# Kernel optimization log

Measured on AMD Instinct MI355X. Metric: run time of the kernel, lower is better.

The kernel has to match this reference:

```python
import jax, jax.numpy as jnp
import numpy as np

WS = 17  # window_size


def _conv(x, w, padding, groups=1):
    return jax.lax.conv_general_dilated(
        x, w, window_strides=(1, 1), padding=padding,
        dimension_numbers=("NCHW", "OIHW", "NCHW"),
        feature_group_count=groups)


def setup_inputs() -> dict:
    key = jax.random.key(0)
    ks = jax.random.split(key, 5)
    B, C, H, W = 4, 64, 510, 510
    x = jax.random.normal(ks[0], (B, C, H, W), dtype=jnp.float32)
    # Sobel depthwise kernel, exactly as init_sobel_weights
    sobel = jnp.array([[-1.0, 0.0, 1.0], [-2.0, 0.0, 2.0], [-1.0, 0.0, 1.0]],
                      dtype=jnp.float32)
    sobel_w = jnp.tile(sobel[None, None], (C, 1, 1, 1))  # [C,1,3,3]
    w1 = jax.random.normal(ks[1], (16, C, 3, 3), jnp.float32) * 0.04
    b1 = jax.random.normal(ks[2], (16,), jnp.float32) * 0.01
    w2 = jax.random.normal(ks[3], (1, 16, 1, 1), jnp.float32) * 0.1
    b2 = jax.random.normal(ks[4], (1,), jnp.float32) * 0.01
    return {"x": x, "sobel_w": sobel_w, "w1": w1, "b1": b1, "w2": w2, "b2": b2}


def reference(x, sobel_w, w1, b1, w2, b2):
    B, C, H, W = x.shape
    pad_h = (-H) % WS
    pad_w = (-W) % WS
    x = jnp.pad(x, ((0, 0), (0, 0), (0, pad_h), (0, pad_w)))
    Hp, Wp = H + pad_h, W + pad_w
    nh, nw = Hp // WS, Wp // WS
    # F.unfold with kernel=stride=WS on NCHW == non-overlapping window split.
    # Window order is row-major over (nh, nw), matching unfold's column order.
    xw = (x.reshape(B, C, nh, WS, nw, WS)
           .transpose(0, 2, 4, 1, 3, 5)
           .reshape(B * nh * nw, C, WS, WS))
    # depthwise 3x3 sobel filter, padding=1
    freq = _conv(xw, sobel_w, [(1, 1), (1, 1)], groups=C)
    # mask generator: Conv(C->16,3x3) + ReLU + Conv(16->1,1x1) + Sigmoid
    h = jax.nn.relu(_conv(freq, w1, [(1, 1), (1, 1)]) + b1[None, :, None, None])
    mask = jax.nn.sigmoid(_conv(h, w2, [(0, 0), (0, 0)]) + b2[None, :, None, None])
    mask = jnp.clip(mask, 0.05, 0.95)
    # F.fold with non-overlapping windows; divisor fold(unfold(ones)) == 1,
    # so the divide / nan_to_num are identities.
    attn = (mask.reshape(B, nh, nw, 1, WS, WS)
                .transpose(0, 3, 1, 4, 2, 5)
                .reshape(B, 1, Hp, Wp))
    return attn[:, :, :H, :W]
```

## Files before the change

### kernel.cpp

```cpp
#include <hip/hip_runtime.h>


#define WSZ 17
#define PS  19
#define PSS (PS * PS)
#define NT  512
#define CH  (510 * 510)

typedef __attribute__((ext_vector_type(8))) short bf16x8;
typedef __attribute__((ext_vector_type(4))) float f32x4;
typedef __attribute__((ext_vector_type(2))) float f32x2;

__device__ __forceinline__ int swz(int off) {
    return off ^ (((off >> 7) & 7) << 4);
}

__device__ __forceinline__ unsigned short f2bf(float f) {
    union { float f; unsigned u; } v; v.f = f;
    unsigned u = v.u;
    unsigned r = u + 0x7fffu + ((u >> 16) & 1u);
    return (unsigned short)(r >> 16);
}

__device__ __forceinline__ float dpp_shr1(float v) {
    return __int_as_float(
        __builtin_amdgcn_update_dpp(0, __float_as_int(v), 0x138, 0xf, 0xf, true));
}
__device__ __forceinline__ float dpp_shl1(float v) {
    return __int_as_float(
        __builtin_amdgcn_update_dpp(0, __float_as_int(v), 0x130, 0xf, 0xf, true));
}

__global__ void prep_w1(const float* __restrict__ w1, unsigned short* __restrict__ wt) {
    const int dij = blockIdx.x >> 1;
    const int ks  = blockIdx.x & 1;
    const int l   = threadIdx.x;
    const int m   = l & 15;
    const int kb  = ks * 32 + 8 * (l >> 4);
    bf16x8 v;
#pragma unroll
    for (int jj = 0; jj < 8; ++jj)
        v[jj] = (short)f2bf(w1[m * 576 + (kb + jj) * 9 + dij]);
    ((bf16x8*)wt)[blockIdx.x * 64 + l] = v;
}

__global__ __launch_bounds__(NT, 4)
void fasa_mfma(const float* __restrict__ x,
               const float* __restrict__ sobel_w,
               const unsigned short* __restrict__ wt,
               const float* __restrict__ b1,
               const float* __restrict__ w2,
               const float* __restrict__ b2,
               float* __restrict__ out)
{
    __shared__ __align__(16) char frq[PSS * 128];

    const int t    = threadIdx.x;
    const int lane = t & 63;
    const int wave = __builtin_amdgcn_readfirstlane(t >> 6);

    const int bid = blockIdx.x;
    const int win = (bid & 7) * 450 + (bid >> 3);
    const int b   = win / 900;
    const int rem = win % 900;
    const int h0  = (rem / 30) * WSZ;
    const int w0  = (rem % 30) * WSZ;

    for (int u = t; u < 72 * 8; u += NT) {
        int r = u >> 3, k = u & 7;
        int row;
        if      (r < 19) row = r;
        else if (r < 38) row = 342 + (r - 19);
        else if (r < 55) row = (r - 37) * PS;
        else             row = (r - 54) * PS + 18;
        *(f32x4*)(frq + row * 128 + k * 16) = (f32x4){0.f, 0.f, 0.f, 0.f};
    }

    float sw[9];
#pragma unroll
    for (int k = 0; k < 9; ++k) sw[k] = sobel_w[k];

    const int j   = lane & 31;
    const int grp = lane >> 5;
    const bool jac = (j < 17);

    const float* xbase = x + ((size_t)(b * 64 + 4 * wave)) * CH
                           + (size_t)h0 * 510 + w0;
    const unsigned voffx = (unsigned)((grp * 2 * CH + j) * 4);
    const unsigned voffy = voffx + (unsigned)(CH * 4);

    auto LOADCOL = [&](f32x2* xr, int q) {
        const char* bp = (const char*)(xbase + (size_t)q * 32 * CH);
        xr[0] = (f32x2){0.f, 0.f}; xr[18] = (f32x2){0.f, 0.f};
        if (jac) {
#pragma unroll
            for (int i = 0; i < 17; ++i) {
                xr[i + 1].x = *(const float*)(bp + (voffx + (unsigned)i * 2040u));
                xr[i + 1].y = *(const float*)(bp + (voffy + (unsigned)i * 2040u));
            }
        } else {
#pragma unroll
            for (int i = 0; i < 17; ++i) xr[i + 1] = (f32x2){0.f, 0.f};
        }
    };

    auto DOSOBEL = [&](const f32x2* xr, int q) {
        const int pr = 2 * wave + grp + 16 * q;
        const int pairOff = pr * 4;
#pragma unroll
        for (int i = 0; i < 17; ++i) {
            f32x2 p0 = sw[0] * xr[i] + sw[3] * xr[i + 1] + sw[6] * xr[i + 2];
            f32x2 p1 = sw[1] * xr[i] + sw[4] * xr[i + 1] + sw[7] * xr[i + 2];
            f32x2 p2 = sw[2] * xr[i] + sw[5] * xr[i + 1] + sw[8] * xr[i + 2];
            f32x2 o;
            o.x = p1.x + dpp_shr1(p0.x) + dpp_shl1(p2.x);
            o.y = p1.y + dpp_shr1(p0.y) + dpp_shl1(p2.y);
            unsigned pkv;
            asm("v_cvt_pk_bf16_f32 %0, %1, %2" : "=v"(pkv) : "v"(o.x), "v"(o.y));
            if (jac)
                *(unsigned*)(frq + swz(((i + 1) * PS + (j + 1)) * 128 + pairOff)) = pkv;
        }
    };

    f32x2 A[19], B[19];
    LOADCOL(A, 0);
    LOADCOL(B, 1);
    DOSOBEL(A, 0);
    DOSOBEL(B, 1);

    bf16x8 wf[18];
#pragma unroll
    for (int i = 0; i < 18; ++i)
        wf[i] = ((const bf16x8*)wt)[i * 64 + lane];

    float b1v[4], w2v[4];
#pragma unroll
    for (int r = 0; r < 4; ++r) {
        int m = 4 * (lane >> 4) + r;
        b1v[r] = b1[m];
        w2v[r] = w2[m];
    }
    const float b2v = b2[0];

    __syncthreads();

    const int n   = lane & 15;
    const int g16 = (lane >> 4) * 16;
    const int DOFF[9] = {0, 1, 2, PS, PS + 1, PS + 2, 2 * PS, 2 * PS + 1, 2 * PS + 2};

#pragma unroll 1
    for (int nt = wave; nt < 19; nt += 8) {
        int p  = nt * 16 + n;
        int pv = p > 288 ? 288 : p;
        int pi = pv / 17, pj = pv - pi * 17;
        int base = (pi * PS + pj) * 128 + g16;

        f32x4 acc = {0.f, 0.f, 0.f, 0.f};
#pragma unroll
        for (int d = 0; d < 9; ++d) {
            int off = base + DOFF[d] * 128;
            bf16x8 bfA = *(const bf16x8*)(frq + swz(off));
            bf16x8 bfB = *(const bf16x8*)(frq + swz(off + 64));
            acc = __builtin_amdgcn_mfma_f32_16x16x32_bf16(wf[2 * d],     bfA, acc, 0, 0, 0);
            acc = __builtin_amdgcn_mfma_f32_16x16x32_bf16(wf[2 * d + 1], bfB, acc, 0, 0, 0);
        }

        float part = 0.f;
#pragma unroll
        for (int r = 0; r < 4; ++r)
            part = fmaf(w2v[r], fmaxf(acc[r] + b1v[r], 0.f), part);
        part += __shfl_xor(part, 16);
        part += __shfl_xor(part, 32);

        if (lane < 16 && p < 289) {
            float pre = part + b2v;
            float s = 1.f / (1.f + expf(-pre));
            s = fminf(fmaxf(s, 0.05f), 0.95f);
            out[((size_t)(b * 510 + h0 + pi)) * 510 + (w0 + pj)] = s;
        }
    }
}

extern "C" void kernel_launch(void* const* d_in, const int* in_sizes, int n_in,
                              void* d_out, int out_size, void* d_ws, size_t ws_size,
                              hipStream_t stream) {
    const float* x       = (const float*)d_in[0];
    const float* sobel_w = (const float*)d_in[1];
    const float* w1      = (const float*)d_in[2];
    const float* b1      = (const float*)d_in[3];
    const float* w2      = (const float*)d_in[4];
    const float* b2      = (const float*)d_in[5];
    float* out = (float*)d_out;
    unsigned short* wtab = (unsigned short*)d_ws;

    prep_w1<<<dim3(18), dim3(64), 0, stream>>>(w1, wtab);
    fasa_mfma<<<dim3(3600), dim3(NT), 0, stream>>>(x, sobel_w, wtab, b1, w2, b2, out);
}
```

Measured before the change: 93.63 us.

## Stage input window via global_load_lds DMA and drop padded frequency tile

Replaces per-lane strided scalar global loads of the 17x17 window with global_load_lds transfers into LDS staging buffers, after which Sobel reads come from LDS. The padded 19x19 frequency tile is replaced by a compact 17x17 tile plus one zero row, with boundary handling moved into the conv loop via index masking. The aim is more efficient global load issue and less zero-initialisation, at the cost of extra barriers, serialised load-then-compute per chunk with no overlap, and more LDS, which may reduce occupancy.

```diff
diff --git a/kernel.cpp b/kernel.cpp
--- a/kernel.cpp
+++ b/kernel.cpp
@@ -2,8 +2,6 @@
 
 
 #define WSZ 17
-#define PS  19
-#define PSS (PS * PS)
 #define NT  512
 #define CH  (510 * 510)
 
@@ -29,6 +27,12 @@
 __device__ __forceinline__ float dpp_shl1(float v) {
     return __int_as_float(
         __builtin_amdgcn_update_dpp(0, __float_as_int(v), 0x130, 0xf, 0xf, true));
+}
+
+typedef __attribute__((address_space(1))) const unsigned GU;
+typedef __attribute__((address_space(3))) unsigned LU;
+__device__ __forceinline__ void gl_lds(const float* g, char* l) {
+    __builtin_amdgcn_global_load_lds((GU*)g, (LU*)l, 4, 0, 0);
 }
 
 __global__ void prep_w1(const float* __restrict__ w1, unsigned short* __restrict__ wt) {
@@ -53,7 +57,9 @@
                const float* __restrict__ b2,
                float* __restrict__ out)
 {
-    __shared__ __align__(16) char frq[PSS * 128];
+    __shared__ __align__(16) char xm[8 * 17 * 256];
+    __shared__ __align__(16) char xt[9 * 256];
+    __shared__ __align__(16) char frq[290 * 128];
 
     const int t    = threadIdx.x;
     const int lane = t & 63;
@@ -66,15 +72,7 @@
     const int h0  = (rem / 30) * WSZ;
     const int w0  = (rem % 30) * WSZ;
 
-    for (int u = t; u < 72 * 8; u += NT) {
-        int r = u >> 3, k = u & 7;
-        int row;
-        if      (r < 19) row = r;
-        else if (r < 38) row = 342 + (r - 19);
-        else if (r < 55) row = (r - 37) * PS;
-        else             row = (r - 54) * PS + 18;
-        *(f32x4*)(frq + row * 128 + k * 16) = (f32x4){0.f, 0.f, 0.f, 0.f};
-    }
+    if (t < 8) *(f32x4*)(frq + 289 * 128 + t * 16) = (f32x4){0.f, 0.f, 0.f, 0.f};
 
     float sw[9];
 #pragma unroll
@@ -84,49 +82,67 @@
     const int grp = lane >> 5;
     const bool jac = (j < 17);
 
-    const float* xbase = x + ((size_t)(b * 64 + 4 * wave)) * CH
-                           + (size_t)h0 * 510 + w0;
-    const unsigned voffx = (unsigned)((grp * 2 * CH + j) * 4);
-    const unsigned voffy = voffx + (unsigned)(CH * 4);
-
-    auto LOADCOL = [&](f32x2* xr, int q) {
-        const char* bp = (const char*)(xbase + (size_t)q * 32 * CH);
-        xr[0] = (f32x2){0.f, 0.f}; xr[18] = (f32x2){0.f, 0.f};
-        if (jac) {
-#pragma unroll
-            for (int i = 0; i < 17; ++i) {
-                xr[i + 1].x = *(const float*)(bp + (voffx + (unsigned)i * 2040u));
-                xr[i + 1].y = *(const float*)(bp + (voffy + (unsigned)i * 2040u));
-            }
-        } else {
-#pragma unroll
-            for (int i = 0; i < 17; ++i) xr[i + 1] = (f32x2){0.f, 0.f};
-        }
+    const float* xw = x + ((size_t)b * 64) * CH + (size_t)h0 * 510 + w0;
+    const float* gm_base = xw + ((size_t)(wave * 4) + (lane >> 4)) * CH + (lane & 15);
+    const float* gt_base = xw + ((size_t)(lane & 31)) * CH + (lane >> 5) * 510 + 16;
+
+    auto DMA_CHUNK = [&](int q) {
+        const float* gm = gm_base + (size_t)q * 32 * CH;
+        char* dm = xm + wave * 17 * 256;
+#pragma unroll
+        for (int i = 0; i < 17; ++i)
+            gl_lds(gm + i * 510, dm + i * 256);
+        const float* gt = gt_base + (size_t)q * 32 * CH;
+        gl_lds(gt + 2 * wave * 510, xt + wave * 256);
+        if (wave == 7)
+            gl_lds(gt + (16 * 510 - (lane >> 5) * 510), xt + 8 * 256);
     };
 
-    auto DOSOBEL = [&](const f32x2* xr, int q) {
-        const int pr = 2 * wave + grp + 16 * q;
-        const int pairOff = pr * 4;
+    auto SOBEL_CHUNK = [&](int q) {
+        const int pr = q * 16 + 2 * wave + grp;
+        const bool j16 = (j == 16);
+        const int mj = j > 15 ? 15 : j;
+        const char* mb = xm + (wave * 17) * 256 + (2 * grp) * 64 + mj * 4;
+        const char* tb = xt + (4 * wave + 2 * grp) * 4;
+        const char* a0 = j16 ? tb : mb;
+        const int st  = j16 ? 128 : 256;
+        const int o2  = j16 ? 4   : 64;
+        f32x2 xr[17];
 #pragma unroll
         for (int i = 0; i < 17; ++i) {
-            f32x2 p0 = sw[0] * xr[i] + sw[3] * xr[i + 1] + sw[6] * xr[i + 2];
-            f32x2 p1 = sw[1] * xr[i] + sw[4] * xr[i + 1] + sw[7] * xr[i + 2];
-            f32x2 p2 = sw[2] * xr[i] + sw[5] * xr[i + 1] + sw[8] * xr[i + 2];
+            float v0 = *(const float*)(a0);
+            float v1 = *(const float*)(a0 + o2);
+            a0 += st;
+            xr[i].x = jac ? v0 : 0.f;
+            xr[i].y = jac ? v1 : 0.f;
+        }
+#pragma unroll
+        for (int i = 0; i < 17; ++i) {
+            f32x2 top = (i > 0)  ? xr[i - 1] : (f32x2){0.f, 0.f};
+            f32x2 mid = xr[i];
+            f32x2 bot = (i < 16) ? xr[i + 1] : (f32x2){0.f, 0.f};
+            f32x2 p0 = sw[0] * top + sw[3] * mid + sw[6] * bot;
+            f32x2 p1 = sw[1] * top + sw[4] * mid + sw[7] * bot;
+            f32x2 p2 = sw[2] * top + sw[5] * mid + sw[8] * bot;
             f32x2 o;
             o.x = p1.x + dpp_shr1(p0.x) + dpp_shl1(p2.x);
             o.y = p1.y + dpp_shr1(p0.y) + dpp_shl1(p2.y);
             unsigned pkv;
             asm("v_cvt_pk_bf16_f32 %0, %1, %2" : "=v"(pkv) : "v"(o.x), "v"(o.y));
             if (jac)
-                *(unsigned*)(frq + swz(((i + 1) * PS + (j + 1)) * 128 + pairOff)) = pkv;
+                *(unsigned*)(frq + swz((i * 17 + j) * 128 + pr * 4)) = pkv;
         }
     };
 
-    f32x2 A[19], B[19];
-    LOADCOL(A, 0);
-    LOADCOL(B, 1);
-    DOSOBEL(A, 0);
-    DOSOBEL(B, 1);
+    DMA_CHUNK(0);
+    asm volatile("s_waitcnt vmcnt(0)" ::: "memory");
+    __syncthreads();
+    SOBEL_CHUNK(0);
+    __syncthreads();
+    DMA_CHUNK(1);
+    asm volatile("s_waitcnt vmcnt(0)" ::: "memory");
+    __syncthreads();
+    SOBEL_CHUNK(1);
 
     bf16x8 wf[18];
 #pragma unroll
@@ -146,19 +162,20 @@
 
     const int n   = lane & 15;
     const int g16 = (lane >> 4) * 16;
-    const int DOFF[9] = {0, 1, 2, PS, PS + 1, PS + 2, 2 * PS, 2 * PS + 1, 2 * PS + 2};
 
 #pragma unroll 1
     for (int nt = wave; nt < 19; nt += 8) {
         int p  = nt * 16 + n;
         int pv = p > 288 ? 288 : p;
         int pi = pv / 17, pj = pv - pi * 17;
-        int base = (pi * PS + pj) * 128 + g16;
 
         f32x4 acc = {0.f, 0.f, 0.f, 0.f};
 #pragma unroll
         for (int d = 0; d < 9; ++d) {
-            int off = base + DOFF[d] * 128;
+            const int di = d / 3 - 1, dj = d % 3 - 1;
+            bool ok = ((unsigned)(pi + di) < 17u) & ((unsigned)(pj + dj) < 17u);
+            int row = ok ? (pv + di * 17 + dj) : 289;
+            int off = row * 128 + g16;
             bf16x8 bfA = *(const bf16x8*)(frq + swz(off));
             bf16x8 bfB = *(const bf16x8*)(frq + swz(off + 64));
             acc = __builtin_amdgcn_mfma_f32_16x16x32_bf16(wf[2 * d],     bfA, acc, 0, 0, 0);
```

After: 117.6 us. 1.26x slower.
